# Kernel optimization log

Hardware: AMD Instinct MI355X
Metric: run time of the kernel (lower is better)

The kernel has to match this reference:

```python
import jax, jax.numpy as jnp
import numpy as np
from jax import lax

# Dimensions (ModelArgs with d_model=1024)
B, L = 2, 1024
D_MODEL = 1024
D_INNER = 2048          # expand * d_model
D_STATE = 16
DT_RANK = 64            # ceil(d_model / 16)
D_CONV = 4


def setup_inputs() -> dict:
    key = jax.random.key(0)
    ks = jax.random.split(key, 8)
    sc = lambda k, shp, s: jax.random.normal(k, shp, dtype=jnp.float32) * s
    x = jax.random.normal(ks[0], (B, L, D_MODEL), dtype=jnp.float32)
    W_in = sc(ks[1], (2 * D_INNER, D_MODEL), 0.02)
    conv_w = sc(ks[2], (D_INNER, D_CONV), 0.2)
    conv_b = jnp.zeros((D_INNER,), jnp.float32)
    W_x = sc(ks[3], (DT_RANK + 2 * D_STATE, D_INNER), 0.02)
    dt_init_std = DT_RANK ** -0.5
    W_dt = jax.random.uniform(ks[4], (D_INNER, DT_RANK), jnp.float32,
                              -dt_init_std, dt_init_std)
    # dt_proj bias: inverse-softplus of dt ~ logUniform(dt_min, dt_max)
    dt_min, dt_max = 1e-3, 1e-1
    u = jax.random.uniform(ks[5], (D_INNER,), jnp.float32)
    dt = jnp.exp(u * (np.log(dt_max) - np.log(dt_min)) + np.log(dt_min))
    dt = jnp.clip(dt, 1e-4, None)
    b_dt = dt + jnp.log(-jnp.expm1(-dt))
    A_log = jnp.log(jnp.tile(jnp.arange(1, D_STATE + 1, dtype=jnp.float32)[None, :],
                             (D_INNER, 1)))
    D = jnp.ones((D_INNER,), jnp.float32)
    W_out = sc(ks[6], (D_MODEL, D_INNER), 0.02)
    return {"x": x, "W_in": W_in, "conv_w": conv_w, "conv_b": conv_b,
            "W_x": W_x, "W_dt": W_dt, "b_dt": b_dt, "A_log": A_log,
            "D": D, "W_out": W_out}


def reference(x, W_in, conv_w, conv_b, W_x, W_dt, b_dt, A_log, D, W_out):
    b, l, _ = x.shape
    d_in, n = A_log.shape
    k = conv_w.shape[1]

    # in_proj, split into conv branch and gating residual
    x_and_res = x @ W_in.T                                 # (b, l, 2*d_in)
    xz, res = jnp.split(x_and_res, [d_in], axis=-1)

    # Causal depthwise conv1d (kernel k, left-pad k-1, truncate to l)
    xp = jnp.pad(xz, ((0, 0), (k - 1, 0), (0, 0)))         # (b, l+k-1, d_in)
    xc = conv_b[None, None, :] + sum(
        xp[:, i:i + l, :] * conv_w[None, None, :, i] for i in range(k))
    xc = jax.nn.silu(xc)                                   # (b, l, d_in)

    # x_proj -> delta, B, C
    x_dbl = xc @ W_x.T                                     # (b, l, dt_rank+2n)
    dlt, Bm, Cm = jnp.split(x_dbl, [DT_RANK, DT_RANK + n], axis=-1)
    delta = jax.nn.softplus(dlt @ W_dt.T + b_dt)           # (b, l, d_in)

    # selective scan
    A = -jnp.exp(A_log)                                    # (d_in, n)
    dA = jnp.exp(delta[..., None] * A[None, None])         # (b, l, d_in, n)
    dBu = (delta * xc)[..., None] * Bm[:, :, None, :]      # (b, l, d_in, n)

    def step(h, inp):
        dA_t, dBu_t, C_t = inp                             # (b,d,n),(b,d,n),(b,n)
        h = dA_t * h + dBu_t
        y = jnp.einsum('bdn,bn->bd', h, C_t)
        return h, y

    h0 = jnp.zeros((b, d_in, n), xc.dtype)
    _, ys = lax.scan(step, h0, (dA.transpose(1, 0, 2, 3),
                                dBu.transpose(1, 0, 2, 3),
                                Cm.transpose(1, 0, 2)))
    y = ys.transpose(1, 0, 2) + xc * D[None, None, :]      # (b, l, d_in)

    y = y * jax.nn.silu(res)
    return y @ W_out.T                                     # (b, l, d_model)
```

## Files before the change

kernel.cpp:

```cpp
#include <hip/hip_runtime.h>
#include <hip/hip_bf16.h>
#include <cmath>

#define DEV __device__ __forceinline__

typedef float  f32x4  __attribute__((ext_vector_type(4)));
typedef __bf16 bf16x8 __attribute__((ext_vector_type(8)));
using u16 = unsigned short;

constexpr int CB   = 2;
constexpr int CLEN = 1024;
constexpr int CDM  = 1024;
constexpr int CDI  = 2048;
constexpr int CM   = CB * CLEN;
constexpr int NCHUNK = 64;
constexpr int CHL    = 16;

DEV u16 f2bf(float f) {
  unsigned u = __builtin_bit_cast(unsigned, f);
  unsigned r = (u + 0x7fffu + ((u >> 16) & 1u)) >> 16;
  return (u16)r;
}

DEV ushort4 f4bf(float4 v) {
  ushort4 o;
  o.x = f2bf(v.x); o.y = f2bf(v.y); o.z = f2bf(v.z); o.w = f2bf(v.w);
  return o;
}

constexpr int CG_X   = 524288;
constexpr int CG_WIN = CG_X   + 1048576;
constexpr int CG_WDT = CG_WIN + 32768;
constexpr int CG_WO  = CG_WDT + 524288;
constexpr int CG_WX  = CG_WO  + 65536;

__global__ void cast_all_k(const float* __restrict__ x, const float* __restrict__ W_in,
                           const float* __restrict__ W_dt, const float* __restrict__ W_out,
                           const float* __restrict__ W_x,
                           u16* __restrict__ xb, u16* __restrict__ W_inb,
                           u16* __restrict__ W_dtb, u16* __restrict__ W_outb,
                           u16* __restrict__ W_xb)
{
  int i = blockIdx.x * blockDim.x + threadIdx.x;
  if (i < CG_X) {
    reinterpret_cast<ushort4*>(xb)[i] = f4bf(reinterpret_cast<const float4*>(x)[i]);
  } else if (i < CG_WIN) {
    int j = i - CG_X;
    reinterpret_cast<ushort4*>(W_inb)[j] = f4bf(reinterpret_cast<const float4*>(W_in)[j]);
  } else if (i < CG_WDT) {
    int j = i - CG_WIN;
    reinterpret_cast<ushort4*>(W_dtb)[j] = f4bf(reinterpret_cast<const float4*>(W_dt)[j]);
  } else if (i < CG_WO) {
    int j = i - CG_WDT;
    reinterpret_cast<ushort4*>(W_outb)[j] = f4bf(reinterpret_cast<const float4*>(W_out)[j]);
  } else {
    int j = i - CG_WO;
    int base = j * 4, row = base >> 11, col = base & 2047;
    float4 v = make_float4(0.f, 0.f, 0.f, 0.f);
    if (row < 96) v = *reinterpret_cast<const float4*>(W_x + row * 2048 + col);
    reinterpret_cast<ushort4*>(W_xb)[j] = f4bf(v);
  }
}

DEV void gload_lds16(const void* g, void* l) {
  __builtin_amdgcn_global_load_lds(
      (const __attribute__((address_space(1))) void*)g,
      (__attribute__((address_space(3))) void*)l, 16, 0, 0);
}

template <int EPI, int SPLITK>
__global__ __launch_bounds__(256, 2)
void gemm_bt(const u16* __restrict__ A, const u16* __restrict__ Bw,
             float* __restrict__ C, const float* __restrict__ bias,
             int Nd, int Kd, int lda, int ldb, int ldc, size_t slice_stride)
{
  __shared__ u16 As[128 * 32];
  __shared__ u16 Bs[128 * 32];
  const int tid  = threadIdx.x;
  const int wave = tid >> 6;
  const int lane = tid & 63;
  const int wm = wave >> 1, wn = wave & 1;
  const int row0 = blockIdx.y * 128;
  const int col0 = blockIdx.x * 128;
  const int lr = lane >> 2;
  const int lc = (lane & 3) * 8;

  const int kper = Kd / SPLITK;
  const int kbeg = (SPLITK > 1) ? blockIdx.z * kper : 0;
  float* Cz = (SPLITK > 1) ? C + (size_t)blockIdx.z * slice_stride : C;

  f32x4 acc[4][4] = {};

  for (int k0 = kbeg; k0 < kbeg + kper; k0 += 32) {
#pragma unroll
    for (int j = 0; j < 2; ++j) {
      const int rb = j * 64 + wave * 16;
      gload_lds16(A  + (size_t)(row0 + rb + lr) * lda + k0 + lc, As + rb * 32);
      gload_lds16(Bw + (size_t)(col0 + rb + lr) * ldb + k0 + lc, Bs + rb * 32);
    }
    __syncthreads();

    const int q  = lane >> 4;
    const int mr = lane & 15;
    bf16x8 af[4], bfr[4];
#pragma unroll
    for (int t = 0; t < 4; ++t) {
      af[t]  = *reinterpret_cast<const bf16x8*>(As + (wm * 64 + t * 16 + mr) * 32 + q * 8);
      bfr[t] = *reinterpret_cast<const bf16x8*>(Bs + (wn * 64 + t * 16 + mr) * 32 + q * 8);
    }
#pragma unroll
    for (int mt = 0; mt < 4; ++mt)
#pragma unroll
      for (int nt = 0; nt < 4; ++nt)
        acc[mt][nt] = __builtin_amdgcn_mfma_f32_16x16x32_bf16(af[mt], bfr[nt], acc[mt][nt], 0, 0, 0);
    __syncthreads();
  }

  const int q  = lane >> 4;
  const int cn = lane & 15;
#pragma unroll
  for (int mt = 0; mt < 4; ++mt)
#pragma unroll
    for (int nt = 0; nt < 4; ++nt)
#pragma unroll
      for (int r = 0; r < 4; ++r) {
        const int row = row0 + wm * 64 + mt * 16 + q * 4 + r;
        const int col = col0 + wn * 64 + nt * 16 + cn;
        float v = acc[mt][nt][r];
        if (EPI == 2) {
          v += bias[col];
          v = (v > 15.f) ? v : log1pf(__expf(v));
        }
        Cz[(size_t)row * ldc + col] = v;
      }
}

__global__ void xdbl_reduce_k(const float* __restrict__ part,
                              float* __restrict__ xdbl, u16* __restrict__ xdblb)
{
  int i = blockIdx.x * blockDim.x + threadIdx.x;
  float4 s = reinterpret_cast<const float4*>(part)[i];
#pragma unroll
  for (int z = 1; z < 8; ++z) {
    float4 p = reinterpret_cast<const float4*>(part + (size_t)z * CM * 128)[i];
    s.x += p.x; s.y += p.y; s.z += p.z; s.w += p.w;
  }
  reinterpret_cast<float4*>(xdbl)[i] = s;
  reinterpret_cast<ushort4*>(xdblb)[i] = f4bf(s);
}

__global__ void conv_silu_k(const float* __restrict__ xz, const float4* __restrict__ cw4,
                            const float* __restrict__ cb,
                            float* __restrict__ xc, u16* __restrict__ xcb)
{
  int idx = blockIdx.x * blockDim.x + threadIdx.x;
  int d   = idx & (CDI - 1);
  int row = idx >> 11;
  int l   = row & (CLEN - 1);
  float4 wv = cw4[d];
  const float* wp = (const float*)&wv;
  float acc = cb[d];
#pragma unroll
  for (int i = 0; i < 4; ++i) {
    int ls = l - 3 + i;
    float v = (ls >= 0) ? xz[(size_t)(row - l + ls) * 4096 + d] : 0.f;
    acc += v * wp[i];
  }
  float s = acc / (1.f + __expf(-acc));
  xc[idx]  = s;
  xcb[idx] = f2bf(s);
}

__global__ __launch_bounds__(256)
void scan_p1(const float* __restrict__ delta, const float* __restrict__ xc,
             const float* __restrict__ xdbl, const float* __restrict__ A_log,
             float* __restrict__ P, float* __restrict__ S)
{
  __shared__ float sB[CHL * 16];
  const int t = threadIdx.x;
  const int d = blockIdx.x * 256 + t;
  const int c = blockIdx.y, b = blockIdx.z;

  if (t < CHL * 16) {
    int ll = t >> 4, n = t & 15;
    sB[t] = xdbl[(size_t)(b * CLEN + c * CHL + ll) * 128 + 64 + n];
  }
  __syncthreads();

  float An[16], Pv[16], Sv[16];
#pragma unroll
  for (int n = 0; n < 16; ++n) {
    An[n] = -__expf(A_log[d * 16 + n]);
    Pv[n] = 1.f; Sv[n] = 0.f;
  }
  const size_t rbase = (size_t)(b * CLEN + c * CHL) * CDI + d;
  for (int ll = 0; ll < CHL; ++ll) {
    float dl = delta[rbase + (size_t)ll * CDI];
    float u  = xc[rbase + (size_t)ll * CDI];
    float du = dl * u;
#pragma unroll
    for (int n = 0; n < 16; ++n) {
      float a = __expf(dl * An[n]);
      Pv[n] *= a;
      Sv[n] = a * Sv[n] + du * sB[ll * 16 + n];
    }
  }
  const size_t o = (size_t)((b * NCHUNK + c) * 16) * CDI + d;
#pragma unroll
  for (int n = 0; n < 16; ++n) {
    P[o + (size_t)n * CDI] = Pv[n];
    S[o + (size_t)n * CDI] = Sv[n];
  }
}

__global__ void scan_p2(const float* __restrict__ P, const float* __restrict__ S,
                        float* __restrict__ Hin)
{
  const int t = threadIdx.x;
  const int d = blockIdx.x * 256 + t;
  const int n = blockIdx.y, b = blockIdx.z;
  float h = 0.f;
#pragma unroll 8
  for (int c = 0; c < NCHUNK; ++c) {
    size_t o = (size_t)((b * NCHUNK + c) * 16 + n) * CDI + d;
    Hin[o] = h;
    h = P[o] * h + S[o];
  }
}

__global__ __launch_bounds__(256)
void scan_p3(const float* __restrict__ delta, const float* __restrict__ xc,
             const float* __restrict__ xdbl, const float* __restrict__ A_log,
             const float* __restrict__ Dvec, const float* __restrict__ xzres,
             const float* __restrict__ Hin, u16* __restrict__ ybarb)
{
  __shared__ float sB[CHL * 16];
  __shared__ float sC[CHL * 16];
  const int t = threadIdx.x;
  const int d = blockIdx.x * 256 + t;
  const int c = blockIdx.y, b = blockIdx.z;

  if (t < CHL * 16) {
    int ll = t >> 4, n = t & 15;
    size_t ro = (size_t)(b * CLEN + c * CHL + ll) * 128;
    sB[t] = xdbl[ro + 64 + n];
    sC[t] = xdbl[ro + 80 + n];
  }
  __syncthreads();

  float An[16], h[16];
  const size_t ho = (size_t)((b * NCHUNK + c) * 16) * CDI + d;
#pragma unroll
  for (int n = 0; n < 16; ++n) {
    An[n] = -__expf(A_log[d * 16 + n]);
    h[n]  = Hin[ho + (size_t)n * CDI];
  }
  const float Dd = Dvec[d];
  const size_t rbase = (size_t)(b * CLEN + c * CHL);
  for (int ll = 0; ll < CHL; ++ll) {
    float dl = delta[(rbase + ll) * CDI + d];
    float u  = xc[(rbase + ll) * CDI + d];
    float du = dl * u;
    float rs = xzres[(rbase + ll) * 4096 + CDI + d];
    float y  = 0.f;
#pragma unroll
    for (int n = 0; n < 16; ++n) {
      float a = __expf(dl * An[n]);
      h[n] = a * h[n] + du * sB[ll * 16 + n];
      y += h[n] * sC[ll * 16 + n];
    }
    y += u * Dd;
    float sr = rs / (1.f + __expf(-rs));
    ybarb[(rbase + ll) * CDI + d] = f2bf(y * sr);
  }
}

extern "C" void kernel_launch(void* const* d_in, const int* in_sizes, int n_in,
                              void* d_out, int out_size, void* d_ws, size_t ws_size,
                              hipStream_t stream)
{
  (void)in_sizes; (void)n_in; (void)out_size; (void)ws_size;
  const float* x      = (const float*)d_in[0];
  const float* W_in   = (const float*)d_in[1];
  const float* conv_w = (const float*)d_in[2];
  const float* conv_b = (const float*)d_in[3];
  const float* W_x    = (const float*)d_in[4];
  const float* W_dt   = (const float*)d_in[5];
  const float* b_dt   = (const float*)d_in[6];
  const float* A_log  = (const float*)d_in[7];
  const float* Dvec   = (const float*)d_in[8];
  const float* W_out  = (const float*)d_in[9];
  float* out = (float*)d_out;

  constexpr size_t MB = 1048576;
  char* w = (char*)d_ws;
  u16*   xb     = (u16*)(w + 0);
  u16*   W_inb  = (u16*)(w + 4 * MB);
  u16*   xcb    = (u16*)(w + 12 * MB);
  u16*   W_xb   = (u16*)(w + 20 * MB);
  u16*   xdblb  = (u16*)(w + 20 * MB + 512 * 1024);
  u16*   W_dtb  = (u16*)(w + 21 * MB);
  float* Pb     = (float*)(w + 0);
  char*  B0     = w + 21 * MB + 256 * 1024;
  float* xpart  = (float*)B0;
  float* Sb     = (float*)B0;
  u16*   ybarb  = (u16*)B0;
  float* Hin    = (float*)(B0 + 16 * MB);
  float* xzres  = (float*)(B0 + 32 * MB);
  float* xc     = (float*)(B0 + 64 * MB);
  float* xdbl   = (float*)(B0 + 80 * MB);
  float* delta  = (float*)(B0 + 81 * MB);
  u16*   W_outb = (u16*)(B0 + 97 * MB);

  dim3 blk(256);
  cast_all_k<<<CG_WX / 256, blk, 0, stream>>>(x, W_in, W_dt, W_out, W_x,
                                              xb, W_inb, W_dtb, W_outb, W_xb);
  gemm_bt<0, 1><<<dim3(32, 16), blk, 0, stream>>>(xb, W_inb, xzres, nullptr,
                                                  4096, 1024, 1024, 1024, 4096, 0);
  conv_silu_k<<<(CB * CLEN * CDI) / 256, blk, 0, stream>>>(xzres, (const float4*)conv_w,
                                                           conv_b, xc, xcb);
  gemm_bt<0, 8><<<dim3(1, 16, 8), blk, 0, stream>>>(xcb, W_xb, xpart, nullptr,
                                                    128, 2048, 2048, 2048, 128,
                                                    (size_t)CM * 128);
  xdbl_reduce_k<<<(CM * 128 / 4) / 256, blk, 0, stream>>>(xpart, xdbl, xdblb);
  gemm_bt<2, 1><<<dim3(16, 16), blk, 0, stream>>>(xdblb, W_dtb, delta, b_dt,
                                                  2048, 64, 128, 64, 2048, 0);
  scan_p1<<<dim3(8, NCHUNK, 2), blk, 0, stream>>>(delta, xc, xdbl, A_log, Pb, Sb);
  scan_p2<<<dim3(8, 16, 2), blk, 0, stream>>>(Pb, Sb, Hin);
  scan_p3<<<dim3(8, NCHUNK, 2), blk, 0, stream>>>(delta, xc, xdbl, A_log, Dvec, xzres,
                                                  Hin, ybarb);
  gemm_bt<0, 1><<<dim3(8, 16), blk, 0, stream>>>(ybarb, W_outb, out, nullptr,
                                                 1024, 2048, 2048, 2048, 1024, 0);
}
```

Before: 260.3 us.

## Store intermediates in bf16, fuse residual silu, split-K the output projection

GEMM epilogues now write bf16 for the in-projection output and delta. The conv kernel precomputes silu of the residual in bf16, and the scan kernels read bf16 delta, xc and gate values instead of fp32. This cuts the global memory traffic of the large activation tensors. The out-projection GEMM is split-K by 4 with a separate reduction kernel to fill more CUs. The trade-off is reduced precision in delta and the activations, plus an extra reduction pass over the output.

```diff
diff --git a/kernel.cpp b/kernel.cpp
--- a/kernel.cpp
+++ b/kernel.cpp
@@ -21,6 +21,7 @@
   unsigned r = (u + 0x7fffu + ((u >> 16) & 1u)) >> 16;
   return (u16)r;
 }
+DEV float bf2f(u16 v) { return __builtin_bit_cast(float, ((unsigned)v) << 16); }
 
 DEV ushort4 f4bf(float4 v) {
   ushort4 o;
@@ -71,7 +72,8 @@
 template <int EPI, int SPLITK>
 __global__ __launch_bounds__(256, 2)
 void gemm_bt(const u16* __restrict__ A, const u16* __restrict__ Bw,
-             float* __restrict__ C, const float* __restrict__ bias,
+             float* __restrict__ C, u16* __restrict__ Cb,
+             const float* __restrict__ bias,
              int Nd, int Kd, int lda, int ldb, int ldc, size_t slice_stride)
 {
   __shared__ u16 As[128 * 32];
@@ -127,11 +129,12 @@
         const int row = row0 + wm * 64 + mt * 16 + q * 4 + r;
         const int col = col0 + wn * 64 + nt * 16 + cn;
         float v = acc[mt][nt][r];
-        if (EPI == 2) {
+        if (EPI == 3) {
           v += bias[col];
           v = (v > 15.f) ? v : log1pf(__expf(v));
         }
-        Cz[(size_t)row * ldc + col] = v;
+        if (EPI == 0) Cz[(size_t)row * ldc + col] = v;
+        else          Cb[(size_t)row * ldc + col] = f2bf(v);
       }
 }
 
@@ -149,9 +152,21 @@
   reinterpret_cast<ushort4*>(xdblb)[i] = f4bf(s);
 }
 
-__global__ void conv_silu_k(const float* __restrict__ xz, const float4* __restrict__ cw4,
+__global__ void out_reduce_k(const float* __restrict__ part, float* __restrict__ out)
+{
+  int i = blockIdx.x * blockDim.x + threadIdx.x;
+  float4 s = reinterpret_cast<const float4*>(part)[i];
+#pragma unroll
+  for (int z = 1; z < 4; ++z) {
+    float4 p = reinterpret_cast<const float4*>(part + (size_t)z * CM * CDM)[i];
+    s.x += p.x; s.y += p.y; s.z += p.z; s.w += p.w;
+  }
+  reinterpret_cast<float4*>(out)[i] = s;
+}
+
+__global__ void conv_silu_k(const u16* __restrict__ xzb, const float4* __restrict__ cw4,
                             const float* __restrict__ cb,
-                            float* __restrict__ xc, u16* __restrict__ xcb)
+                            u16* __restrict__ xcb, u16* __restrict__ rsb)
 {
   int idx = blockIdx.x * blockDim.x + threadIdx.x;
   int d   = idx & (CDI - 1);
@@ -163,16 +178,17 @@
 #pragma unroll
   for (int i = 0; i < 4; ++i) {
     int ls = l - 3 + i;
-    float v = (ls >= 0) ? xz[(size_t)(row - l + ls) * 4096 + d] : 0.f;
+    float v = (ls >= 0) ? bf2f(xzb[(size_t)(row - l + ls) * 4096 + d]) : 0.f;
     acc += v * wp[i];
   }
   float s = acc / (1.f + __expf(-acc));
-  xc[idx]  = s;
   xcb[idx] = f2bf(s);
+  float r = bf2f(xzb[(size_t)row * 4096 + CDI + d]);
+  rsb[idx] = f2bf(r / (1.f + __expf(-r)));
 }
 
 __global__ __launch_bounds__(256)
-void scan_p1(const float* __restrict__ delta, const float* __restrict__ xc,
+void scan_p1(const u16* __restrict__ delta_b, const u16* __restrict__ xcb,
              const float* __restrict__ xdbl, const float* __restrict__ A_log,
              float* __restrict__ P, float* __restrict__ S)
 {
@@ -195,8 +211,8 @@
   }
   const size_t rbase = (size_t)(b * CLEN + c * CHL) * CDI + d;
   for (int ll = 0; ll < CHL; ++ll) {
-    float dl = delta[rbase + (size_t)ll * CDI];
-    float u  = xc[rbase + (size_t)ll * CDI];
+    float dl = bf2f(delta_b[rbase + (size_t)ll * CDI]);
+    float u  = bf2f(xcb[rbase + (size_t)ll * CDI]);
     float du = dl * u;
 #pragma unroll
     for (int n = 0; n < 16; ++n) {
@@ -229,9 +245,9 @@
 }
 
 __global__ __launch_bounds__(256)
-void scan_p3(const float* __restrict__ delta, const float* __restrict__ xc,
+void scan_p3(const u16* __restrict__ delta_b, const u16* __restrict__ xcb,
              const float* __restrict__ xdbl, const float* __restrict__ A_log,
-             const float* __restrict__ Dvec, const float* __restrict__ xzres,
+             const float* __restrict__ Dvec, const u16* __restrict__ rsb,
              const float* __restrict__ Hin, u16* __restrict__ ybarb)
 {
   __shared__ float sB[CHL * 16];
@@ -258,10 +274,10 @@
   const float Dd = Dvec[d];
   const size_t rbase = (size_t)(b * CLEN + c * CHL);
   for (int ll = 0; ll < CHL; ++ll) {
-    float dl = delta[(rbase + ll) * CDI + d];
-    float u  = xc[(rbase + ll) * CDI + d];
+    size_t e = (rbase + ll) * CDI + d;
+    float dl = bf2f(delta_b[e]);
+    float u  = bf2f(xcb[e]);
     float du = dl * u;
-    float rs = xzres[(rbase + ll) * 4096 + CDI + d];
     float y  = 0.f;
 #pragma unroll
     for (int n = 0; n < 16; ++n) {
@@ -270,8 +286,7 @@
       y += h[n] * sC[ll * 16 + n];
     }
     y += u * Dd;
-    float sr = rs / (1.f + __expf(-rs));
-    ybarb[(rbase + ll) * CDI + d] = f2bf(y * sr);
+    ybarb[e] = f2bf(y * bf2f(rsb[e]));
   }
 }
 
@@ -294,41 +309,43 @@
 
   constexpr size_t MB = 1048576;
   char* w = (char*)d_ws;
-  u16*   xb     = (u16*)(w + 0);
-  u16*   W_inb  = (u16*)(w + 4 * MB);
-  u16*   xcb    = (u16*)(w + 12 * MB);
-  u16*   W_xb   = (u16*)(w + 20 * MB);
-  u16*   xdblb  = (u16*)(w + 20 * MB + 512 * 1024);
-  u16*   W_dtb  = (u16*)(w + 21 * MB);
-  float* Pb     = (float*)(w + 0);
-  char*  B0     = w + 21 * MB + 256 * 1024;
-  float* xpart  = (float*)B0;
-  float* Sb     = (float*)B0;
-  u16*   ybarb  = (u16*)B0;
-  float* Hin    = (float*)(B0 + 16 * MB);
-  float* xzres  = (float*)(B0 + 32 * MB);
-  float* xc     = (float*)(B0 + 64 * MB);
-  float* xdbl   = (float*)(B0 + 80 * MB);
-  float* delta  = (float*)(B0 + 81 * MB);
-  u16*   W_outb = (u16*)(B0 + 97 * MB);
+  u16*   xzres_b = (u16*)(w + 0);
+  u16*   xb      = (u16*)(w + 16 * MB);
+  u16*   W_inb   = (u16*)(w + 20 * MB);
+  float* xpart   = (float*)(w + 28 * MB);
+  float* opart   = (float*)(w + 0);
+  float* Pb      = (float*)(w + 36 * MB);
+  float* Sb      = (float*)(w + 52 * MB);
+  float* Hin     = (float*)(w + 68 * MB);
+  u16*   xcb     = (u16*)(w + 84 * MB);
+  u16*   rsb     = (u16*)(w + 92 * MB);
+  float* xdbl    = (float*)(w + 100 * MB);
+  u16*   xdblb   = (u16*)(w + 101 * MB);
+  u16*   W_xb    = (u16*)(w + 101 * MB + 512 * 1024);
+  u16*   W_dtb   = (u16*)(w + 102 * MB);
+  u16*   delta_b = (u16*)(w + 102 * MB + 256 * 1024);
+  u16*   ybarb   = (u16*)(w + 110 * MB + 256 * 1024);
+  u16*   W_outb  = (u16*)(w + 118 * MB + 256 * 1024);
 
   dim3 blk(256);
   cast_all_k<<<CG_WX / 256, blk, 0, stream>>>(x, W_in, W_dt, W_out, W_x,
                                               xb, W_inb, W_dtb, W_outb, W_xb);
-  gemm_bt<0, 1><<<dim3(32, 16), blk, 0, stream>>>(xb, W_inb, xzres, nullptr,
+  gemm_bt<1, 1><<<dim3(32, 16), blk, 0, stream>>>(xb, W_inb, nullptr, xzres_b, nullptr,
                                                   4096, 1024, 1024, 1024, 4096, 0);
-  conv_silu_k<<<(CB * CLEN * CDI) / 256, blk, 0, stream>>>(xzres, (const float4*)conv_w,
-                                                           conv_b, xc, xcb);
-  gemm_bt<0, 8><<<dim3(1, 16, 8), blk, 0, stream>>>(xcb, W_xb, xpart, nullptr,
+  conv_silu_k<<<(CB * CLEN * CDI) / 256, blk, 0, stream>>>(xzres_b, (const float4*)conv_w,
+                                                           conv_b, xcb, rsb);
+  gemm_bt<0, 8><<<dim3(1, 16, 8), blk, 0, stream>>>(xcb, W_xb, xpart, nullptr, nullptr,
                                                     128, 2048, 2048, 2048, 128,
                                                     (size_t)CM * 128);
   xdbl_reduce_k<<<(CM * 128 / 4) / 256, blk, 0, stream>>>(xpart, xdbl, xdblb);
-  gemm_bt<2, 1><<<dim3(16, 16), blk, 0, stream>>>(xdblb, W_dtb, delta, b_dt,
+  gemm_bt<3, 1><<<dim3(16, 16), blk, 0, stream>>>(xdblb, W_dtb, nullptr, delta_b, b_dt,
                                                   2048, 64, 128, 64, 2048, 0);
-  scan_p1<<<dim3(8, NCHUNK, 2), blk, 0, stream>>>(delta, xc, xdbl, A_log, Pb, Sb);
+  scan_p1<<<dim3(8, NCHUNK, 2), blk, 0, stream>>>(delta_b, xcb, xdbl, A_log, Pb, Sb);
   scan_p2<<<dim3(8, 16, 2), blk, 0, stream>>>(Pb, Sb, Hin);
-  scan_p3<<<dim3(8, NCHUNK, 2), blk, 0, stream>>>(delta, xc, xdbl, A_log, Dvec, xzres,
+  scan_p3<<<dim3(8, NCHUNK, 2), blk, 0, stream>>>(delta_b, xcb, xdbl, A_log, Dvec, rsb,
                                                   Hin, ybarb);
-  gemm_bt<0, 1><<<dim3(8, 16), blk, 0, stream>>>(ybarb, W_outb, out, nullptr,
-                                                 1024, 2048, 2048, 2048, 1024, 0);
-}
+  gemm_bt<0, 4><<<dim3(8, 16, 4), blk, 0, stream>>>(ybarb, W_outb, opart, nullptr, nullptr,
+                                                    1024, 2048, 2048, 2048, 1024,
+                                                    (size_t)CM * CDM);
+  out_reduce_k<<<(CM * CDM / 4) / 256, blk, 0, stream>>>(opart, out);
+}
```

Result: faster. 254.1 us (-2.4%).
